# Performance work log

Hardware: AMD Instinct MI355X
Metric: run time of the kernel (lower is better)

Reference implementation:

```python
import jax, jax.numpy as jnp
import numpy as np

B, L, D_MODEL = 2, 2048, 1024
N_HEADS, D_K = 16, 64  # d_v == d_k (required by the output*q epilogue)


def setup_inputs() -> dict:
    key = jax.random.key(0)
    ks = jax.random.split(key, 8)
    # xavier_normal std for [d_model, d_k] fan: sqrt(2/(d_model+d_k))
    std = float(np.sqrt(2.0 / (D_MODEL + D_K)))
    std_p = float(np.sqrt(1.0 / (N_HEADS * D_K)))  # nn.Linear default ~ U(-1/sqrt(fan_in),..); normal approx ok for a baseline
    return {
        "q": jax.random.normal(ks[0], (B, L, D_MODEL), jnp.float32),
        "k": jax.random.normal(ks[1], (B, L, D_MODEL), jnp.float32),
        "v": jax.random.normal(ks[2], (B, L, D_MODEL), jnp.float32),
        "w_qs": jax.random.normal(ks[3], (N_HEADS, D_MODEL, D_K), jnp.float32) * std,
        "w_ks": jax.random.normal(ks[4], (N_HEADS, D_MODEL, D_K), jnp.float32) * std,
        "w_vs": jax.random.normal(ks[5], (N_HEADS, D_MODEL, D_K), jnp.float32) * std,
        "w_proj": jax.random.normal(ks[6], (D_MODEL, N_HEADS * D_K), jnp.float32) * std_p,
        "b_proj": jnp.zeros((D_MODEL,), jnp.float32),
    }


def reference(q, k, v, w_qs, w_ks, w_vs, w_proj, b_proj):
    # Per-head projections: [h, B, L, d_k]
    qh = jnp.einsum("bld,hdk->hblk", q, w_qs)
    kh = jnp.einsum("bld,hdk->hblk", k, w_ks)
    vh = jnp.einsum("bld,hdk->hblk", v, w_vs)
    # UNscaled attention (no 1/sqrt(d_k)), dropout is identity at eval
    attn = jax.nn.softmax(jnp.einsum("hblk,hbmk->hblm", qh, kh), axis=-1)
    # attn @ V with elementwise *q epilogue
    out = jnp.einsum("hblm,hbmk->hblk", attn, vh) * qh
    # torch.cat(torch.split(outputs, mb_size, 0), -1): heads concat on last dim
    out = out.transpose(1, 2, 0, 3).reshape(q.shape[0], q.shape[1], -1)  # [B, L, h*d_k]
    return out @ w_proj.T + b_proj
```

## Files before the change

kernel.cpp:

```cpp
#include <hip/hip_runtime.h>

#define B_ 2
#define L_ 2048
#define DM 1024
#define H_ 16
#define DK 64
#define ROWS (B_*L_)
#define BK 32
#define LDT 40

typedef _Float16 f16x8 __attribute__((ext_vector_type(8)));
typedef float    f32x4 __attribute__((ext_vector_type(4)));
typedef unsigned short us8 __attribute__((ext_vector_type(8)));
typedef unsigned short us4v __attribute__((ext_vector_type(4)));

__device__ __forceinline__ unsigned short f2h(float f) {
    _Float16 h = (_Float16)f;
    return __builtin_bit_cast(unsigned short, h);
}
__device__ __forceinline__ float h2f(unsigned short u) {
    return (float)__builtin_bit_cast(_Float16, u);
}
__device__ __forceinline__ f16x8 ld8h(const unsigned short* p) {
    return *reinterpret_cast<const f16x8*>(p);
}
__device__ __forceinline__ us8 cvt_us8(float4 a, float4 b) {
    us8 u;
    u[0] = f2h(a.x); u[1] = f2h(a.y); u[2] = f2h(a.z); u[3] = f2h(a.w);
    u[4] = f2h(b.x); u[5] = f2h(b.y); u[6] = f2h(b.z); u[7] = f2h(b.w);
    return u;
}

#define MFMA(a, b, c) __builtin_amdgcn_mfma_f32_16x16x32_f16((a), (b), (c), 0, 0, 0)

#define AS1 __attribute__((address_space(1)))
#define AS3 __attribute__((address_space(3)))
__device__ __forceinline__ void glds16(const void* g, void* l) {
    __builtin_amdgcn_global_load_lds((const AS1 unsigned int*)g,
                                     (AS3 unsigned int*)l, 16, 0, 0);
}

__global__ __launch_bounds__(256) void kcvt(
    const float* __restrict__ src, unsigned short* __restrict__ dst)
{
    size_t i = ((size_t)blockIdx.x * 256 + threadIdx.x) * 8;
    const float4* s4 = (const float4*)(src + i);
    *(us8*)(dst + i) = cvt_us8(s4[0], s4[1]);
}

__global__ __launch_bounds__(256) void kcvt3(
    const float* __restrict__ q, const float* __restrict__ k,
    const float* __restrict__ v, unsigned short* __restrict__ dst)
{
    int bx = blockIdx.x;
    int which = bx >> 11, rem = bx & 2047;
    const float* src = (which == 0) ? q : (which == 1) ? k : v;
    size_t i = ((size_t)rem * 256 + threadIdx.x) * 8;
    const float4* s4 = (const float4*)(src + i);
    *(us8*)(dst + (size_t)which * ROWS * DM + i) = cvt_us8(s4[0], s4[1]);
}

__global__ __launch_bounds__(256) void k0_transpose_w(
    const float* __restrict__ wq,
    const float* __restrict__ wk,
    const float* __restrict__ wv,
    unsigned short* __restrict__ wt)
{
    __shared__ unsigned short tile[64][65];
    int bx = blockIdx.x;
    int which = bx / (H_ * 16);
    int rem   = bx % (H_ * 16);
    int h  = rem >> 4;
    int db = (rem & 15) * 64;
    const float* src = (which == 0) ? wq : (which == 1) ? wk : wv;
    float scale = (which == 1) ? 1.44269504f : 1.0f;

    int t = threadIdx.x;
    int r = t >> 2;
    int c = (t & 3) * 16;
    const float4* sp = (const float4*)(src + ((size_t)(h * DM + db + r)) * DK + c);
    #pragma unroll
    for (int i4 = 0; i4 < 4; i4++) {
        float4 f = sp[i4];
        tile[r][c + i4 * 4 + 0] = f2h(f.x * scale);
        tile[r][c + i4 * 4 + 1] = f2h(f.y * scale);
        tile[r][c + i4 * 4 + 2] = f2h(f.z * scale);
        tile[r][c + i4 * 4 + 3] = f2h(f.w * scale);
    }
    __syncthreads();

    int n   = t >> 2;
    int d16 = (t & 3) * 16;
    __align__(16) unsigned short ov[16];
    #pragma unroll
    for (int i = 0; i < 16; i++) ov[i] = tile[d16 + i][n];
    size_t off = (((size_t)which * H_ + h) * DK + n) * DM + db + d16;
    *(us8*)(wt + off)     = *(us8*)&ov[0];
    *(us8*)(wt + off + 8) = *(us8*)&ov[8];
}

__global__ __launch_bounds__(256) void k1_proj_fp16(
    const unsigned short* __restrict__ qkvh,
    const unsigned short* __restrict__ wt,
    unsigned short* __restrict__ qh,
    unsigned short* __restrict__ kh,
    unsigned short* __restrict__ vt)
{
    __shared__ __align__(16) unsigned short sA[128 * BK];
    __shared__ __align__(16) unsigned short sB[128 * BK];

    int bx = blockIdx.x;
    int which = bx >> 8;
    int rem   = bx & 255;
    int mbase = (rem >> 3) * 128;
    int nbase = (rem & 7) * 128;

    const unsigned short* Ag = qkvh + (size_t)which * ROWS * DM;
    const unsigned short* Bg = wt + (size_t)which * DM * DM;

    int t = threadIdx.x;
    int wave = t >> 6, lane = t & 63, quad = lane >> 4, l16 = lane & 15;
    int wm = (wave >> 1) * 64, wn = (wave & 1) * 64;

    const unsigned short* gA0 = Ag + (size_t)(mbase + (t >> 2)) * DM + (t & 3) * 8;
    const unsigned short* gA1 = gA0 + (size_t)64 * DM;
    const unsigned short* gB0 = Bg + (size_t)(nbase + (t >> 2)) * DM + (t & 3) * 8;
    const unsigned short* gB1 = gB0 + (size_t)64 * DM;
    unsigned short* lA0 = &sA[(size_t)t * 8];
    unsigned short* lA1 = &sA[(size_t)(256 + t) * 8];
    unsigned short* lB0 = &sB[(size_t)t * 8];
    unsigned short* lB1 = &sB[(size_t)(256 + t) * 8];

    f32x4 acc[4][4];
    #pragma unroll
    for (int mi = 0; mi < 4; mi++)
        #pragma unroll
        for (int ni = 0; ni < 4; ni++) acc[mi][ni] = (f32x4)0.0f;

    for (int step = 0; step < 32; step++) {
        if (step) __syncthreads();
        glds16(gA0, lA0); glds16(gA1, lA1);
        glds16(gB0, lB0); glds16(gB1, lB1);
        gA0 += BK; gA1 += BK; gB0 += BK; gB1 += BK;
        __syncthreads();

        f16x8 aF[4], bF[4];
        #pragma unroll
        for (int mi = 0; mi < 4; mi++)
            aF[mi] = *(const f16x8*)&sA[(wm + mi * 16 + l16) * BK + quad * 8];
        #pragma unroll
        for (int ni = 0; ni < 4; ni++)
            bF[ni] = *(const f16x8*)&sB[(wn + ni * 16 + l16) * BK + quad * 8];
        __builtin_amdgcn_s_setprio(1);
        #pragma unroll
        for (int mi = 0; mi < 4; mi++)
            #pragma unroll
            for (int ni = 0; ni < 4; ni++)
                acc[mi][ni] = MFMA(aF[mi], bF[ni], acc[mi][ni]);
        __builtin_amdgcn_s_setprio(0);
    }

    int h = (nbase >> 6) + (wave & 1);
    if (which < 2) {
        unsigned short* OUT = ((which == 0) ? qh : kh) + (size_t)h * ROWS * DK;
        #pragma unroll
        for (int mi = 0; mi < 4; mi++)
            #pragma unroll
            for (int ni = 0; ni < 4; ni++)
                #pragma unroll
                for (int r = 0; r < 4; r++) {
                    int row = mbase + wm + mi * 16 + quad * 4 + r;
                    OUT[(size_t)row * DK + ni * 16 + l16] = f2h(acc[mi][ni][r]);
                }
    } else {
        unsigned short* OUT = vt + (size_t)h * DK * ROWS;
        #pragma unroll
        for (int mi = 0; mi < 4; mi++)
            #pragma unroll
            for (int ni = 0; ni < 4; ni++) {
                int dk   = ni * 16 + l16;
                int rowb = mbase + wm + mi * 16 + quad * 4;
                us4v pk;
                pk[0] = f2h(acc[mi][ni][0]); pk[1] = f2h(acc[mi][ni][1]);
                pk[2] = f2h(acc[mi][ni][2]); pk[3] = f2h(acc[mi][ni][3]);
                *(us4v*)(OUT + (size_t)dk * ROWS + rowb) = pk;
            }
    }
}

__global__ __launch_bounds__(256) void k1_proj_qkv(
    const float* __restrict__ q,
    const float* __restrict__ k,
    const float* __restrict__ v,
    const unsigned short* __restrict__ wt,
    unsigned short* __restrict__ qh,
    unsigned short* __restrict__ kh,
    unsigned short* __restrict__ vt)
{
    __shared__ __align__(16) unsigned short sA[128 * LDT];
    __shared__ __align__(16) unsigned short sB[128 * LDT];

    int bx = blockIdx.x;
    int which = bx >> 8;
    int rem   = bx & 255;
    int mbase = (rem >> 3) * 128;
    int nbase = (rem & 7) * 128;

    const float* Ag = (which == 0) ? q : (which == 1) ? k : v;
    const unsigned short* Bg = wt + (size_t)which * DM * DM;

    int t = threadIdx.x;
    int wave = t >> 6, lane = t & 63, quad = lane >> 4, l16 = lane & 15;
    int wm = (wave >> 1) * 64, wn = (wave & 1) * 64;

    int ar0 = t >> 2,         ac0 = t & 3;
    int ar1 = (256 + t) >> 2, ac1 = t & 3;
    const float* pA0 = Ag + (size_t)(mbase + ar0) * DM + ac0 * 8;
    const float* pA1 = Ag + (size_t)(mbase + ar1) * DM + ac1 * 8;
    const unsigned short* pB0 = Bg + (size_t)(nbase + ar0) * DM + ac0 * 8;
    const unsigned short* pB1 = Bg + (size_t)(nbase + ar1) * DM + ac1 * 8;
    unsigned short* wA0 = &sA[ar0 * LDT + ac0 * 8];
    unsigned short* wA1 = &sA[ar1 * LDT + ac1 * 8];
    unsigned short* wB0 = &sB[ar0 * LDT + ac0 * 8];
    unsigned short* wB1 = &sB[ar1 * LDT + ac1 * 8];

    f32x4 acc[4][4];
    #pragma unroll
    for (int mi = 0; mi < 4; mi++)
        #pragma unroll
        for (int ni = 0; ni < 4; ni++) acc[mi][ni] = (f32x4)0.0f;

    float4 rA0a = *(const float4*)pA0, rA0b = *(const float4*)(pA0 + 4);
    float4 rA1a = *(const float4*)pA1, rA1b = *(const float4*)(pA1 + 4);
    us8 rB0 = *(const us8*)pB0, rB1 = *(const us8*)pB1;

    for (int step = 0; step < 32; step++) {
        if (step) __syncthreads();
        *(us8*)wA0 = cvt_us8(rA0a, rA0b);
        *(us8*)wA1 = cvt_us8(rA1a, rA1b);
        *(us8*)wB0 = rB0; *(us8*)wB1 = rB1;
        __syncthreads();
        if (step < 31) {
            pA0 += BK; pA1 += BK; pB0 += BK; pB1 += BK;
            rA0a = *(const float4*)pA0; rA0b = *(const float4*)(pA0 + 4);
            rA1a = *(const float4*)pA1; rA1b = *(const float4*)(pA1 + 4);
            rB0 = *(const us8*)pB0; rB1 = *(const us8*)pB1;
        }
        f16x8 aF[4], bF[4];
        #pragma unroll
        for (int mi = 0; mi < 4; mi++)
            aF[mi] = *(const f16x8*)&sA[(wm + mi * 16 + l16) * LDT + quad * 8];
        #pragma unroll
        for (int ni = 0; ni < 4; ni++)
            bF[ni] = *(const f16x8*)&sB[(wn + ni * 16 + l16) * LDT + quad * 8];
        #pragma unroll
        for (int mi = 0; mi < 4; mi++)
            #pragma unroll
            for (int ni = 0; ni < 4; ni++)
                acc[mi][ni] = MFMA(aF[mi], bF[ni], acc[mi][ni]);
    }

    int h = (nbase >> 6) + (wave & 1);
    if (which < 2) {
        unsigned short* OUT = ((which == 0) ? qh : kh) + (size_t)h * ROWS * DK;
        #pragma unroll
        for (int mi = 0; mi < 4; mi++)
            #pragma unroll
            for (int ni = 0; ni < 4; ni++)
                #pragma unroll
                for (int r = 0; r < 4; r++) {
                    int row = mbase + wm + mi * 16 + quad * 4 + r;
                    OUT[(size_t)row * DK + ni * 16 + l16] = f2h(acc[mi][ni][r]);
                }
    } else {
        unsigned short* OUT = vt + (size_t)h * DK * ROWS;
        #pragma unroll
        for (int mi = 0; mi < 4; mi++)
            #pragma unroll
            for (int ni = 0; ni < 4; ni++) {
                int dk   = ni * 16 + l16;
                int rowb = mbase + wm + mi * 16 + quad * 4;
                us4v pk;
                pk[0] = f2h(acc[mi][ni][0]); pk[1] = f2h(acc[mi][ni][1]);
                pk[2] = f2h(acc[mi][ni][2]); pk[3] = f2h(acc[mi][ni][3]);
                *(us4v*)(OUT + (size_t)dk * ROWS + rowb) = pk;
            }
    }
}

__global__ __launch_bounds__(256) void k2_attn(
    const unsigned short* __restrict__ qh,
    const unsigned short* __restrict__ kh,
    const unsigned short* __restrict__ vt,
    unsigned short* __restrict__ x2)
{
    __shared__ __align__(16) unsigned short ktile[64][72];
    __shared__ __align__(16) unsigned short vtile[64][72];
    __shared__ __align__(16) unsigned short pld[4][16][72];

    int bx = blockIdx.x;
    int xcd = bx & 7;
    int loc = bx >> 3;
    int hb  = xcd * 4 + (loc >> 5);
    int qt  = loc & 31;
    int h = hb >> 1, b = hb & 1;
    int qbase = qt * 64;

    const unsigned short* qhp = qh + ((size_t)h * ROWS + b * L_) * DK;
    const unsigned short* khp = kh + ((size_t)h * ROWS + b * L_) * DK;
    const unsigned short* vtp = vt + (size_t)h * DK * ROWS + b * L_;

    int wave = threadIdx.x >> 6, lane = threadIdx.x & 63;
    int quad = lane >> 4, l16 = lane & 15;
    int t = threadIdx.x;

    int qrow = qbase + wave * 16 + l16;
    f16x8 qb0 = ld8h(qhp + (size_t)qrow * DK + quad * 8);
    f16x8 qb1 = ld8h(qhp + (size_t)qrow * DK + 32 + quad * 8);

    float m_i = -1e30f, l_i = 0.0f;
    f32x4 o[4];
    #pragma unroll
    for (int nt = 0; nt < 4; nt++) o[nt] = (f32x4)0.0f;

    for (int kt = 0; kt < 32; kt++) {
        int kb = kt * 64;
        {
            const unsigned short* kg = khp + (size_t)kb * DK;
            #pragma unroll
            for (int i = 0; i < 2; i++) {
                int c = i * 256 + t;
                int key = c >> 3, ch = (c & 7) * 8;
                *(us8*)&ktile[key][ch] = *(const us8*)(kg + c * 8);
            }
            #pragma unroll
            for (int i = 0; i < 2; i++) {
                int c = i * 256 + t;
                int dk = c >> 3, ch = (c & 7) * 8;
                *(us8*)&vtile[dk][ch] = *(const us8*)(vtp + (size_t)dk * ROWS + kb + ch);
            }
        }
        __syncthreads();

        f32x4 s[4];
        #pragma unroll
        for (int nt = 0; nt < 4; nt++) s[nt] = (f32x4)0.0f;
        __builtin_amdgcn_s_setprio(1);
        #pragma unroll
        for (int nt = 0; nt < 4; nt++) {
            f16x8 ka0 = *(const f16x8*)&ktile[nt * 16 + l16][quad * 8];
            f16x8 ka1 = *(const f16x8*)&ktile[nt * 16 + l16][32 + quad * 8];
            s[nt] = MFMA(ka0, qb0, s[nt]);
            s[nt] = MFMA(ka1, qb1, s[nt]);
        }
        __builtin_amdgcn_s_setprio(0);

        float pm[4];
        #pragma unroll
        for (int nt = 0; nt < 4; nt++) {
            float a = fmaxf(s[nt][0], s[nt][1]);
            float c2 = fmaxf(s[nt][2], s[nt][3]);
            pm[nt] = fmaxf(a, c2);
        }
        float mx = fmaxf(fmaxf(pm[0], pm[1]), fmaxf(pm[2], pm[3]));
        mx = fmaxf(mx, __shfl_xor(mx, 16));
        mx = fmaxf(mx, __shfl_xor(mx, 32));

        if (!__all(mx - m_i <= 11.0f)) {
            float mnew  = fmaxf(m_i, mx);
            float alpha = __builtin_amdgcn_exp2f(m_i - mnew);
            l_i *= alpha;
            #pragma unroll
            for (int r = 0; r < 4; r++) {
                float av = __shfl(alpha, quad * 4 + r);
                #pragma unroll
                for (int nt = 0; nt < 4; nt++) o[nt][r] *= av;
            }
            m_i = mnew;
        }

        float ps[4];
        #pragma unroll
        for (int nt = 0; nt < 4; nt++) {
            float e0 = __builtin_amdgcn_exp2f(s[nt][0] - m_i);
            float e1 = __builtin_amdgcn_exp2f(s[nt][1] - m_i);
            float e2 = __builtin_amdgcn_exp2f(s[nt][2] - m_i);
            float e3 = __builtin_amdgcn_exp2f(s[nt][3] - m_i);
            s[nt][0] = e0; s[nt][1] = e1; s[nt][2] = e2; s[nt][3] = e3;
            ps[nt] = (e0 + e1) + (e2 + e3);
        }
        float rs = (ps[0] + ps[1]) + (ps[2] + ps[3]);
        rs += __shfl_xor(rs, 16);
        rs += __shfl_xor(rs, 32);
        l_i += rs;

        #pragma unroll
        for (int nt = 0; nt < 4; nt++) {
            us4v pk;
            pk[0] = f2h(s[nt][0]); pk[1] = f2h(s[nt][1]);
            pk[2] = f2h(s[nt][2]); pk[3] = f2h(s[nt][3]);
            *(us4v*)&pld[wave][l16][nt * 16 + quad * 4] = pk;
        }

        __builtin_amdgcn_s_setprio(1);
        #pragma unroll
        for (int kk = 0; kk < 2; kk++) {
            f16x8 pa = *(const f16x8*)&pld[wave][l16][kk * 32 + quad * 8];
            #pragma unroll
            for (int nt = 0; nt < 4; nt++) {
                f16x8 vb = *(const f16x8*)&vtile[nt * 16 + l16][kk * 32 + quad * 8];
                o[nt] = MFMA(pa, vb, o[nt]);
            }
        }
        __builtin_amdgcn_s_setprio(0);
        __syncthreads();
    }

    float linv = 1.0f / l_i;
    #pragma unroll
    for (int r = 0; r < 4; r++) {
        float lv = __shfl(linv, quad * 4 + r);
        int row = qbase + wave * 16 + quad * 4 + r;
        #pragma unroll
        for (int nt = 0; nt < 4; nt++) {
            int col = nt * 16 + l16;
            float qv = h2f(qhp[(size_t)row * DK + col]);
            float val = o[nt][r] * lv * qv;
            x2[((size_t)b * L_ + row) * DM + h * DK + col] = f2h(val);
        }
    }
}

__global__ __launch_bounds__(256) void k3_out_proj(
    const unsigned short* __restrict__ x2,
    const unsigned short* __restrict__ wph,
    const float* __restrict__ bias,
    float* __restrict__ out)
{
    __shared__ __align__(16) unsigned short sA[128 * BK];
    __shared__ __align__(16) unsigned short sB[128 * BK];

    int bx = blockIdx.x;
    int mbase = (bx >> 3) * 128;
    int nbase = (bx & 7) * 128;

    int t = threadIdx.x;
    int wave = t >> 6, lane = t & 63, quad = lane >> 4, l16 = lane & 15;
    int wm = (wave >> 1) * 64, wn = (wave & 1) * 64;

    const unsigned short* gA0 = x2 + (size_t)(mbase + (t >> 2)) * DM + (t & 3) * 8;
    const unsigned short* gA1 = gA0 + (size_t)64 * DM;
    const unsigned short* gB0 = wph + (size_t)(nbase + (t >> 2)) * DM + (t & 3) * 8;
    const unsigned short* gB1 = gB0 + (size_t)64 * DM;
    unsigned short* lA0 = &sA[(size_t)t * 8];
    unsigned short* lA1 = &sA[(size_t)(256 + t) * 8];
    unsigned short* lB0 = &sB[(size_t)t * 8];
    unsigned short* lB1 = &sB[(size_t)(256 + t) * 8];

    f32x4 acc[4][4];
    #pragma unroll
    for (int mi = 0; mi < 4; mi++)
        #pragma unroll
        for (int ni = 0; ni < 4; ni++) acc[mi][ni] = (f32x4)0.0f;

    for (int step = 0; step < 32; step++) {
        if (step) __syncthreads();
        glds16(gA0, lA0); glds16(gA1, lA1);
        glds16(gB0, lB0); glds16(gB1, lB1);
        gA0 += BK; gA1 += BK; gB0 += BK; gB1 += BK;
        __syncthreads();

        f16x8 aF[4], bF[4];
        #pragma unroll
        for (int mi = 0; mi < 4; mi++)
            aF[mi] = *(const f16x8*)&sA[(wm + mi * 16 + l16) * BK + quad * 8];
        #pragma unroll
        for (int ni = 0; ni < 4; ni++)
            bF[ni] = *(const f16x8*)&sB[(wn + ni * 16 + l16) * BK + quad * 8];
        __builtin_amdgcn_s_setprio(1);
        #pragma unroll
        for (int mi = 0; mi < 4; mi++)
            #pragma unroll
            for (int ni = 0; ni < 4; ni++)
                acc[mi][ni] = MFMA(aF[mi], bF[ni], acc[mi][ni]);
        __builtin_amdgcn_s_setprio(0);
    }

    float bv[4];
    #pragma unroll
    for (int ni = 0; ni < 4; ni++) bv[ni] = bias[nbase + wn + ni * 16 + l16];

    #pragma unroll
    for (int mi = 0; mi < 4; mi++)
        #pragma unroll
        for (int ni = 0; ni < 4; ni++)
            #pragma unroll
            for (int r = 0; r < 4; r++) {
                int row = mbase + wm + mi * 16 + quad * 4 + r;
                int col = nbase + wn + ni * 16 + l16;
                out[(size_t)row * DM + col] = acc[mi][ni][r] + bv[ni];
            }
}

extern "C" void kernel_launch(void* const* d_in, const int* in_sizes, int n_in,
                              void* d_out, int out_size, void* d_ws, size_t ws_size,
                              hipStream_t stream)
{
    const float* q     = (const float*)d_in[0];
    const float* k     = (const float*)d_in[1];
    const float* v     = (const float*)d_in[2];
    const float* wqs   = (const float*)d_in[3];
    const float* wks   = (const float*)d_in[4];
    const float* wvs   = (const float*)d_in[5];
    const float* wproj = (const float*)d_in[6];
    const float* bproj = (const float*)d_in[7];
    float* out = (float*)d_out;

    char* ws = (char*)d_ws;
    #define MB (size_t)(1024 * 1024)
    unsigned short* wt   = (unsigned short*)(ws);
    unsigned short* wph  = (unsigned short*)(ws + 6  * MB);
    unsigned short* qh   = (unsigned short*)(ws + 8  * MB);
    unsigned short* kh   = (unsigned short*)(ws + 16 * MB);
    unsigned short* vt   = (unsigned short*)(ws + 24 * MB);
    unsigned short* x2   = (unsigned short*)(ws + 32 * MB);
    unsigned short* qkvh = (unsigned short*)(ws + 32 * MB);

    kcvt<<<dim3((DM * DM) / (256 * 8)), dim3(256), 0, stream>>>(wproj, wph);
    k0_transpose_w<<<dim3(3 * H_ * 16), dim3(256), 0, stream>>>(wqs, wks, wvs, wt);

    if (ws_size >= 56 * MB) {
        kcvt3<<<dim3(3 * 2048), dim3(256), 0, stream>>>(q, k, v, qkvh);
        k1_proj_fp16<<<dim3(3 * 32 * 8), dim3(256), 0, stream>>>(qkvh, wt, qh, kh, vt);
    } else {
        k1_proj_qkv<<<dim3(3 * 32 * 8), dim3(256), 0, stream>>>(q, k, v, wt, qh, kh, vt);
    }
    k2_attn<<<dim3(H_ * B_ * 32), dim3(256), 0, stream>>>(qh, kh, vt, x2);
    k3_out_proj<<<dim3(32 * 8), dim3(256), 0, stream>>>(x2, wph, bproj, out);
}
```

Measured before the change: 255.4 us.

## Double-buffer K/V tiles with direct global-to-LDS loads and XOR swizzle

The attention kernel now keeps two K/V shared-memory buffers and prefetches the next key tile with direct global-to-LDS loads while it computes on the current one. This removes the synchronous register-staged load before each compute step. It also drops the padded LDS rows in favour of an XOR swizzle on K, V and the P staging buffer to avoid bank conflicts. The cost is doubled LDS for K/V and a reliance on correct wait and barrier ordering for the asynchronous loads.

New measurement: 249.1 us. 2.5% less time.

```diff
diff --git a/kernel.cpp b/kernel.cpp
--- a/kernel.cpp
+++ b/kernel.cpp
@@ -294,9 +294,9 @@
     const unsigned short* __restrict__ vt,
     unsigned short* __restrict__ x2)
 {
-    __shared__ __align__(16) unsigned short ktile[64][72];
-    __shared__ __align__(16) unsigned short vtile[64][72];
-    __shared__ __align__(16) unsigned short pld[4][16][72];
+    __shared__ __align__(16) unsigned short ktile[2][64][64];
+    __shared__ __align__(16) unsigned short vtile[2][64][64];
+    __shared__ __align__(16) unsigned short pld[4][16][64];
 
     int bx = blockIdx.x;
     int xcd = bx & 7;
@@ -313,6 +313,21 @@
     int wave = threadIdx.x >> 6, lane = threadIdx.x & 63;
     int quad = lane >> 4, l16 = lane & 15;
     int t = threadIdx.x;
+    int g8 = (l16 & 7) * 8;
+
+    int c0 = t,       key0 = c0 >> 3, ss0 = ((c0 & 7) ^ (key0 & 7)) * 8;
+    int c1 = 256 + t, key1 = c1 >> 3, ss1 = ((c1 & 7) ^ (key1 & 7)) * 8;
+    const unsigned short* kg0 = khp + (size_t)key0 * DK + ss0;
+    const unsigned short* kg1 = khp + (size_t)key1 * DK + ss1;
+    const unsigned short* vg0 = vtp + (size_t)key0 * ROWS + ss0;
+    const unsigned short* vg1 = vtp + (size_t)key1 * ROWS + ss1;
+    unsigned short* kl0[2] = { &ktile[0][0][0] + c0 * 8, &ktile[1][0][0] + c0 * 8 };
+    unsigned short* kl1[2] = { &ktile[0][0][0] + c1 * 8, &ktile[1][0][0] + c1 * 8 };
+    unsigned short* vl0[2] = { &vtile[0][0][0] + c0 * 8, &vtile[1][0][0] + c0 * 8 };
+    unsigned short* vl1[2] = { &vtile[0][0][0] + c1 * 8, &vtile[1][0][0] + c1 * 8 };
+
+    glds16(kg0, kl0[0]); glds16(kg1, kl1[0]);
+    glds16(vg0, vl0[0]); glds16(vg1, vl1[0]);
 
     int qrow = qbase + wave * 16 + l16;
     f16x8 qb0 = ld8h(qhp + (size_t)qrow * DK + quad * 8);
@@ -323,24 +338,17 @@
     #pragma unroll
     for (int nt = 0; nt < 4; nt++) o[nt] = (f32x4)0.0f;
 
+    __syncthreads();
+
+    int cur = 0;
     for (int kt = 0; kt < 32; kt++) {
-        int kb = kt * 64;
-        {
-            const unsigned short* kg = khp + (size_t)kb * DK;
-            #pragma unroll
-            for (int i = 0; i < 2; i++) {
-                int c = i * 256 + t;
-                int key = c >> 3, ch = (c & 7) * 8;
-                *(us8*)&ktile[key][ch] = *(const us8*)(kg + c * 8);
-            }
-            #pragma unroll
-            for (int i = 0; i < 2; i++) {
-                int c = i * 256 + t;
-                int dk = c >> 3, ch = (c & 7) * 8;
-                *(us8*)&vtile[dk][ch] = *(const us8*)(vtp + (size_t)dk * ROWS + kb + ch);
-            }
-        }
-        __syncthreads();
+        if (kt < 31) {
+            size_t ko = (size_t)(kt + 1) * 64 * DK;
+            size_t vo = (size_t)(kt + 1) * 64;
+            int nb = cur ^ 1;
+            glds16(kg0 + ko, kl0[nb]); glds16(kg1 + ko, kl1[nb]);
+            glds16(vg0 + vo, vl0[nb]); glds16(vg1 + vo, vl1[nb]);
+        }
 
         f32x4 s[4];
         #pragma unroll
@@ -348,8 +356,9 @@
         __builtin_amdgcn_s_setprio(1);
         #pragma unroll
         for (int nt = 0; nt < 4; nt++) {
-            f16x8 ka0 = *(const f16x8*)&ktile[nt * 16 + l16][quad * 8];
-            f16x8 ka1 = *(const f16x8*)&ktile[nt * 16 + l16][32 + quad * 8];
+            const unsigned short* kr = &ktile[cur][nt * 16 + l16][0];
+            f16x8 ka0 = *(const f16x8*)(kr + ((quad * 8) ^ g8));
+            f16x8 ka1 = *(const f16x8*)(kr + ((32 + quad * 8) ^ g8));
             s[nt] = MFMA(ka0, qb0, s[nt]);
             s[nt] = MFMA(ka1, qb1, s[nt]);
         }
@@ -399,21 +408,24 @@
             us4v pk;
             pk[0] = f2h(s[nt][0]); pk[1] = f2h(s[nt][1]);
             pk[2] = f2h(s[nt][2]); pk[3] = f2h(s[nt][3]);
-            *(us4v*)&pld[wave][l16][nt * 16 + quad * 4] = pk;
+            *(us4v*)&pld[wave][l16][(nt * 16 + quad * 4) ^ g8] = pk;
         }
 
         __builtin_amdgcn_s_setprio(1);
         #pragma unroll
         for (int kk = 0; kk < 2; kk++) {
-            f16x8 pa = *(const f16x8*)&pld[wave][l16][kk * 32 + quad * 8];
+            f16x8 pa = *(const f16x8*)&pld[wave][l16][(kk * 32 + quad * 8) ^ g8];
             #pragma unroll
             for (int nt = 0; nt < 4; nt++) {
-                f16x8 vb = *(const f16x8*)&vtile[nt * 16 + l16][kk * 32 + quad * 8];
+                const unsigned short* vr = &vtile[cur][nt * 16 + l16][0];
+                f16x8 vb = *(const f16x8*)(vr + ((kk * 32 + quad * 8) ^ g8));
                 o[nt] = MFMA(pa, vb, o[nt]);
             }
         }
         __builtin_amdgcn_s_setprio(0);
+
         __syncthreads();
+        cur ^= 1;
     }
 
     float linv = 1.0f / l_i;
```
